# Optimization experiments

Measured on AMD Instinct MI355X. Metric: run time of the kernel, lower is better.

Reference implementation:

```python
import jax, jax.numpy as jnp
import numpy as np
from jax import lax

B, T, V, E, H, K = 128, 512, 100000, 100, 128, 12
HD = H // 2
START, STOP = 10, 11
NEG = -10000.0


def setup_inputs() -> dict:
    key = jax.random.key(0)
    ks = jax.random.split(key, 16)
    sentences = jax.random.randint(ks[0], (B, T), 0, V)
    embed = jax.random.normal(ks[1], (V, E), dtype=jnp.float32) * 0.1
    s = 1.0 / np.sqrt(HD).astype(np.float32)
    def u(k, shape):
        return jax.random.uniform(k, shape, minval=-s, maxval=s, dtype=jnp.float32)
    W_ih_f = u(ks[2], (4 * HD, E)); W_hh_f = u(ks[3], (4 * HD, HD))
    b_ih_f = u(ks[4], (4 * HD,));   b_hh_f = u(ks[5], (4 * HD,))
    W_ih_b = u(ks[6], (4 * HD, E)); W_hh_b = u(ks[7], (4 * HD, HD))
    b_ih_b = u(ks[8], (4 * HD,));   b_hh_b = u(ks[9], (4 * HD,))
    W_out = u(ks[10], (K, H)); b_out = u(ks[11], (K,))
    transitions = jax.random.normal(ks[12], (K, K), dtype=jnp.float32)
    transitions = transitions.at[:, START].set(NEG).at[STOP, :].set(NEG)
    h0 = jax.random.normal(ks[13], (2, B, HD), dtype=jnp.float32)
    c0 = jax.random.normal(ks[14], (2, B, HD), dtype=jnp.float32)
    return dict(sentences=sentences, embed=embed,
                W_ih_f=W_ih_f, W_hh_f=W_hh_f, b_ih_f=b_ih_f, b_hh_f=b_hh_f,
                W_ih_b=W_ih_b, W_hh_b=W_hh_b, b_ih_b=b_ih_b, b_hh_b=b_hh_b,
                W_out=W_out, b_out=b_out, transitions=transitions, h0=h0, c0=c0)


def _lstm_dir(x, h, c, Wih, Whh, bih, bhh):
    # x: [B,T,E] -> pre-gates [B,T,4HD] (input projection done once, outside scan)
    xg = jnp.einsum('bte,ge->btg', x, Wih) + bih + bhh
    def step(carry, xt):
        h, c = carry
        g = xt + h @ Whh.T                      # [B,4HD], gate order i,f,g,o (PyTorch)
        i, f, gg, o = jnp.split(g, 4, axis=-1)
        c = jax.nn.sigmoid(f) * c + jax.nn.sigmoid(i) * jnp.tanh(gg)
        h = jax.nn.sigmoid(o) * jnp.tanh(c)
        return (h, c), h
    _, hs = lax.scan(step, (h, c), jnp.swapaxes(xg, 0, 1))  # [T,B,HD]
    return jnp.swapaxes(hs, 0, 1)


def reference(sentences, embed, W_ih_f, W_hh_f, b_ih_f, b_hh_f,
              W_ih_b, W_hh_b, b_ih_b, b_hh_b, W_out, b_out,
              transitions, h0, c0):
    emb = embed[sentences]                       # [B,T,E]
    out_f = _lstm_dir(emb, h0[0], c0[0], W_ih_f, W_hh_f, b_ih_f, b_hh_f)
    out_b = _lstm_dir(emb[:, ::-1], h0[1], c0[1], W_ih_b, W_hh_b, b_ih_b, b_hh_b)[:, ::-1]
    feats = jnp.concatenate([out_f, out_b], axis=-1)   # [B,T,H]
    emissions = feats @ W_out.T + b_out                # [B,T,K]

    def viterbi(em):                                   # em: [T,K]
        def step(prev, e_t):
            v = prev[:, None] + transitions            # [K,K]: from-tag rows, to-tag cols
            return e_t + jnp.max(v, axis=0), jnp.argmax(v, axis=0)
        last, bps = lax.scan(step, em[0], em[1:])      # trellis[0] = emissions[0]
        score = jnp.max(last)
        start = jnp.argmax(last)
        def back(cur, bp):
            return bp[cur], cur                        # emit tag at t, carry tag at t-1
        tag0, tail = lax.scan(back, start, bps, reverse=True)
        path = jnp.concatenate([tag0[None], tail])     # [T]
        return score, path

    scores, paths = jax.vmap(viterbi)(emissions)
    return scores, paths
```

## Files before the change

### kernel.cpp

```cpp
#include <hip/hip_runtime.h>
#include <hip/hip_bf16.h>

#define Bn 128
#define Tn 512
#define En 100
#define G4 256
#define Hn 128
#define Kn 12

typedef short bf16x8 __attribute__((ext_vector_type(8)));
typedef float f32x4 __attribute__((ext_vector_type(4)));

__device__ __forceinline__ void wg_barrier() {
  asm volatile("s_waitcnt lgkmcnt(0)" ::: "memory");
  __builtin_amdgcn_s_barrier();
  asm volatile("" ::: "memory");
}

__device__ __forceinline__ float exp2_hw(float x) {
  float r; asm("v_exp_f32 %0, %1" : "=v"(r) : "v"(x)); return r;
}
__device__ __forceinline__ float rcp_hw(float x) {
  float r; asm("v_rcp_f32 %0, %1" : "=v"(r) : "v"(x)); return r;
}
__device__ __forceinline__ float fast_tanh(float x) {
  return 1.0f - 2.0f * rcp_hw(1.0f + exp2_hw(x * 2.8853900817779268f));
}
__device__ __forceinline__ unsigned int pk2bf(float a, float b) {
  unsigned int ua = __float_as_uint(a); ua += 0x7FFFu + ((ua >> 16) & 1u);
  unsigned int ub = __float_as_uint(b); ub += 0x7FFFu + ((ub >> 16) & 1u);
  return (ua >> 16) | (ub & 0xFFFF0000u);
}

__global__ __launch_bounds__(256) void proj_kernel(
    const int* __restrict__ sent, const float* __restrict__ embed,
    const float* __restrict__ WihF, const float* __restrict__ WihB,
    const float* __restrict__ bihF, const float* __restrict__ bhhF,
    const float* __restrict__ bihB, const float* __restrict__ bhhB,
    float* __restrict__ xgF, float* __restrict__ xgB, int dirSel) {
  __shared__ __align__(16) unsigned short embS[64][128];
  __shared__ __align__(16) unsigned short wS[128][128];
  __shared__ float bias_s[128];
  const int tid = threadIdx.x;
  const int nhalf = blockIdx.y;
  const int dir = (dirSel >= 0) ? dirSel : (int)blockIdx.z;
  const float* Wih = dir ? WihB : WihF;
  const float* bih = dir ? bihB : bihF;
  const float* bhh = dir ? bhhB : bhhF;
  float* xg = dir ? xgB : xgF;
  const int n0 = blockIdx.x * 64;
  const int g0 = nhalf * 128;
  {
    const int t = tid >> 2, q = tid & 3;
    const int row = sent[n0 + t];
    const float* er = embed + (size_t)row * En;
    for (int c = q; c < 16; c += 4) {
      uint4 wv;
      if (c < 12) {
        const float4 f0 = *(const float4*)(er + 8 * c);
        const float4 f1 = *(const float4*)(er + 8 * c + 4);
        wv = make_uint4(pk2bf(f0.x, f0.y), pk2bf(f0.z, f0.w),
                        pk2bf(f1.x, f1.y), pk2bf(f1.z, f1.w));
      } else if (c == 12) {
        float f[8];
#pragma unroll
        for (int j = 0; j < 8; ++j) { const int e = 96 + j; f[j] = (e < En) ? er[e] : 0.f; }
        wv = make_uint4(pk2bf(f[0], f[1]), pk2bf(f[2], f[3]),
                        pk2bf(f[4], f[5]), pk2bf(f[6], f[7]));
      } else {
        wv = make_uint4(0, 0, 0, 0);
      }
      *(uint4*)&embS[t][8 * (c ^ (t & 7))] = wv;
    }
  }
  {
    const int r = tid >> 1, q = tid & 1;
    const float* wr = Wih + (size_t)(g0 + r) * En;
    for (int c = q; c < 16; c += 2) {
      uint4 wv;
      if (c < 12) {
        const float4 f0 = *(const float4*)(wr + 8 * c);
        const float4 f1 = *(const float4*)(wr + 8 * c + 4);
        wv = make_uint4(pk2bf(f0.x, f0.y), pk2bf(f0.z, f0.w),
                        pk2bf(f1.x, f1.y), pk2bf(f1.z, f1.w));
      } else if (c == 12) {
        float f[8];
#pragma unroll
        for (int j = 0; j < 8; ++j) { const int e = 96 + j; f[j] = (e < En) ? wr[e] : 0.f; }
        wv = make_uint4(pk2bf(f[0], f[1]), pk2bf(f[2], f[3]),
                        pk2bf(f[4], f[5]), pk2bf(f[6], f[7]));
      } else {
        wv = make_uint4(0, 0, 0, 0);
      }
      *(uint4*)&wS[r][8 * (c ^ (r & 7))] = wv;
    }
  }
  if (tid < 128) bias_s[tid] = bih[g0 + tid] + bhh[g0 + tid];
  __syncthreads();
  const int m = tid >> 6;
  const int lane = tid & 63;
  const int lr = lane & 15;
  const int lq = lane >> 4;
  const int t = 16 * m + lr;
  f32x4 acc[8] = {};
#pragma unroll
  for (int ks = 0; ks < 4; ++ks) {
    const int cs = 4 * ks + lq;
    const bf16x8 af = *(const bf16x8*)&embS[t][8 * (cs ^ (lr & 7))];
#pragma unroll
    for (int nt = 0; nt < 8; ++nt) {
      const int g = 16 * nt + lr;
      const bf16x8 bf = *(const bf16x8*)&wS[g][8 * (cs ^ (lr & 7))];
      acc[nt] = __builtin_amdgcn_mfma_f32_16x16x32_bf16(af, bf, acc[nt], 0, 0, 0);
    }
  }
  float* xbase = xg + (size_t)(n0 + 16 * m) * G4 + g0;
#pragma unroll
  for (int nt = 0; nt < 8; ++nt) {
    const int g = 16 * nt + lr;
    const float bv = bias_s[g];
#pragma unroll
    for (int j = 0; j < 4; ++j) {
      const int tok = 4 * lq + j;
      xbase[(size_t)tok * G4 + g] = acc[nt][j] + bv;
    }
  }
}

__global__ __launch_bounds__(512, 2) void lstm_kernel(
    const float* __restrict__ xgF, const float* __restrict__ xgB,
    const float* __restrict__ WhhF, const float* __restrict__ WhhB,
    const float* __restrict__ h0, const float* __restrict__ c0,
    float* __restrict__ feats, int dirSel) {
  __shared__ __align__(16) float h_s[2][64];
  int d, b;
  if (dirSel < 0) { d = blockIdx.x >> 7; b = blockIdx.x & 127; }
  else            { d = dirSel;          b = blockIdx.x; }
  const int tid = threadIdx.x;
  const int lane = tid & 63;
  const int w = tid >> 6;
  const int kh = lane >> 5;
  const int gt = (lane >> 3) & 3;
  const int u = lane & 7;
  const int unit = 8 * w + u;
  const int row = gt * 64 + unit;
  const float* xg = d ? xgB : xgF;
  const float* Whh = d ? WhhB : WhhF;
  float a00,a01,a02,a03,a04,a05,a06,a07,a08,a09,a10,a11,a12,a13,a14,a15,
        a16,a17,a18,a19,a20,a21,a22,a23,a24,a25,a26,a27,a28,a29,a30,a31;
  {
    const float4* wp = (const float4*)(Whh + (size_t)row * 64 + 32 * kh);
    const float4 w0 = wp[0], w1 = wp[1], w2 = wp[2], w3 = wp[3];
    const float4 w4 = wp[4], w5 = wp[5], w6 = wp[6], w7 = wp[7];
#define ST(A, V) asm volatile("v_accvgpr_write_b32 %0, %1" : "=a"(A) : "v"(V))
    ST(a00, w0.x); ST(a01, w0.y); ST(a02, w0.z); ST(a03, w0.w);
    ST(a04, w1.x); ST(a05, w1.y); ST(a06, w1.z); ST(a07, w1.w);
    ST(a08, w2.x); ST(a09, w2.y); ST(a10, w2.z); ST(a11, w2.w);
    ST(a12, w3.x); ST(a13, w3.y); ST(a14, w3.z); ST(a15, w3.w);
    ST(a16, w4.x); ST(a17, w4.y); ST(a18, w4.z); ST(a19, w4.w);
    ST(a20, w5.x); ST(a21, w5.y); ST(a22, w5.z); ST(a23, w5.w);
    ST(a24, w6.x); ST(a25, w6.y); ST(a26, w6.z); ST(a27, w6.w);
    ST(a28, w7.x); ST(a29, w7.y); ST(a30, w7.z); ST(a31, w7.w);
#undef ST
  }
  const bool isT = (gt == 2);
  const float fA = isT ? 1.0f : 0.0f;
  const float fB = isT ? -2.0f : 1.0f;
  const float fC = isT ? 2.8853900817779268f : -1.4426950408889634f;
  float c = 0.f;
  if (lane < 8) {
    c = c0[(size_t)d * (Bn * 64) + (size_t)b * 64 + unit];
    h_s[0][unit] = h0[(size_t)d * (Bn * 64) + (size_t)b * 64 + unit];
  }
  const float* xb = xg + (size_t)b * Tn * G4 + row;
  float* fbase = feats + (size_t)b * Tn * Hn + d * 64 + unit;
  const int t0 = d ? (Tn - 1) : 0;
  const int ts = d ? -1 : 1;
  float p0 = 0.f, p1 = 0.f, p2 = 0.f, p3 = 0.f;
  if (kh == 0) {
    p0 = xb[(size_t)t0 * G4];
    p1 = xb[(size_t)(t0 + ts) * G4];
    p2 = xb[(size_t)(t0 + 2 * ts) * G4];
    p3 = xb[(size_t)(t0 + 3 * ts) * G4];
  }

#define ARD8(U0,U1,U2,U3,U4,U5,U6,U7, A0,A1,A2,A3,A4,A5,A6,A7)                \
  asm volatile("v_accvgpr_read_b32 %0, %8\n\t"                                \
               "v_accvgpr_read_b32 %1, %9\n\t"                                \
               "v_accvgpr_read_b32 %2, %10\n\t"                               \
               "v_accvgpr_read_b32 %3, %11\n\t"                               \
               "v_accvgpr_read_b32 %4, %12\n\t"                               \
               "v_accvgpr_read_b32 %5, %13\n\t"                               \
               "v_accvgpr_read_b32 %6, %14\n\t"                               \
               "v_accvgpr_read_b32 %7, %15"                                   \
               : "=&v"(U0),"=&v"(U1),"=&v"(U2),"=&v"(U3),                     \
                 "=&v"(U4),"=&v"(U5),"=&v"(U6),"=&v"(U7)                      \
               : "a"(A0),"a"(A1),"a"(A2),"a"(A3),                             \
                 "a"(A4),"a"(A5),"a"(A6),"a"(A7))
#define F4(HV, U0, U1, U2, U3)                                                 \
    s0 = fmaf((HV).x, U0, s0); s1 = fmaf((HV).y, U1, s1);                      \
    s2 = fmaf((HV).z, U2, s2); s3 = fmaf((HV).w, U3, s3);

#define LSTM_STEP(P, TT, RB) do {                                              \
    wg_barrier();                                                              \
    const float4* hp = (const float4*)(&h_s[RB][32 * kh]);                     \
    const float4 h0v = hp[0], h1v = hp[1], h2v = hp[2], h3v = hp[3];           \
    const float4 h4v = hp[4], h5v = hp[5], h6v = hp[6], h7v = hp[7];           \
    float u00,u01,u02,u03,u04,u05,u06,u07,u08,u09,u10,u11,u12,u13,u14,u15,     \
          u16,u17,u18,u19,u20,u21,u22,u23,u24,u25,u26,u27,u28,u29,u30,u31;     \
    ARD8(u00,u01,u02,u03,u04,u05,u06,u07, a00,a01,a02,a03,a04,a05,a06,a07);    \
    ARD8(u08,u09,u10,u11,u12,u13,u14,u15, a08,a09,a10,a11,a12,a13,a14,a15);    \
    ARD8(u16,u17,u18,u19,u20,u21,u22,u23, a16,a17,a18,a19,a20,a21,a22,a23);    \
    ARD8(u24,u25,u26,u27,u28,u29,u30,u31, a24,a25,a26,a27,a28,a29,a30,a31);    \
    float s0 = 0.f, s1 = 0.f, s2 = 0.f, s3 = 0.f;                              \
    F4(h0v, u00,u01,u02,u03)                                                   \
    F4(h1v, u04,u05,u06,u07)                                                   \
    F4(h2v, u08,u09,u10,u11)                                                   \
    F4(h3v, u12,u13,u14,u15)                                                   \
    F4(h4v, u16,u17,u18,u19)                                                   \
    F4(h5v, u20,u21,u22,u23)                                                   \
    F4(h6v, u24,u25,u26,u27)                                                   \
    F4(h7v, u28,u29,u30,u31)                                                   \
    const float smine = (s0 + s1) + (s2 + s3);                                 \
    const float stot = smine + __shfl_xor(smine, 32);                          \
    const float accv = (P) + stot;                                             \
    const float act = fmaf(fB, rcp_hw(1.0f + exp2_hw(fC * accv)), fA);         \
    const float gF = __shfl_xor(act, 8);                                       \
    const float gG = __shfl_xor(act, 16);                                      \
    const float gO = __shfl_xor(act, 24);                                      \
    if (lane < 8) {                                                            \
      c = fmaf(gF, c, act * gG);                                               \
      const float hh = gO * fast_tanh(c);                                      \
      h_s[RB ^ 1][unit] = hh;                                                  \
      fbase[(size_t)(TT) * Hn] = hh;                                           \
    }                                                                          \
  } while (0)

  for (int s = 0; s < Tn; s += 4) {
    const int tA = t0 + s * ts;
    LSTM_STEP(p0, tA, 0);
    if (kh == 0 && s + 4 < Tn) p0 = xb[(size_t)(t0 + (s + 4) * ts) * G4];
    LSTM_STEP(p1, tA + ts, 1);
    if (kh == 0 && s + 5 < Tn) p1 = xb[(size_t)(t0 + (s + 5) * ts) * G4];
    LSTM_STEP(p2, tA + 2 * ts, 0);
    if (kh == 0 && s + 6 < Tn) p2 = xb[(size_t)(t0 + (s + 6) * ts) * G4];
    LSTM_STEP(p3, tA + 3 * ts, 1);
    if (kh == 0 && s + 7 < Tn) p3 = xb[(size_t)(t0 + (s + 7) * ts) * G4];
  }
#undef LSTM_STEP
#undef F4
#undef ARD8
}

__global__ __launch_bounds__(256) void emis_kernel(
    const float* __restrict__ feats, const float* __restrict__ Wout,
    const float* __restrict__ bout, float* __restrict__ em) {
  __shared__ __align__(16) float Wo[Kn * Hn];
  __shared__ float bo[Kn];
  const int tid = threadIdx.x;
  for (int i = tid; i < Kn * Hn; i += 256) Wo[i] = Wout[i];
  if (tid < Kn) bo[tid] = bout[tid];
  __syncthreads();
  const int n = blockIdx.x * 256 + tid;
  float acc[Kn];
#pragma unroll
  for (int k = 0; k < Kn; ++k) acc[k] = bo[k];
  const float4* fp = (const float4*)(feats + (size_t)n * Hn);
#pragma unroll 4
  for (int d4 = 0; d4 < 32; ++d4) {
    const float4 v = fp[d4];
#pragma unroll
    for (int k = 0; k < Kn; ++k) {
      const float4 w = *(const float4*)&Wo[k * Hn + d4 * 4];
      acc[k] = fmaf(v.x, w.x, acc[k]);
      acc[k] = fmaf(v.y, w.y, acc[k]);
      acc[k] = fmaf(v.z, w.z, acc[k]);
      acc[k] = fmaf(v.w, w.w, acc[k]);
    }
  }
  float* ep = em + (size_t)n * Kn;
#pragma unroll
  for (int k = 0; k < Kn; k += 4)
    *(float4*)&ep[k] = make_float4(acc[k], acc[k + 1], acc[k + 2], acc[k + 3]);
}

#define AMAX(v, a, v2, a2) { if ((v2) > (v)) { (v) = (v2); (a) = (a2); } }

__global__ __launch_bounds__(64) void viterbi_kernel(
    const float* __restrict__ em, const float* __restrict__ trans,
    float* __restrict__ out) {
  __shared__ __align__(16) float em_s[Tn * Kn];
  __shared__ float trans_s[Kn * Kn];
  __shared__ unsigned char bp[(Tn - 1) * Kn];
  __shared__ short path_s[Tn];
  const int tid = threadIdx.x;
  const int b = blockIdx.x;
  {
    const float4* ebv = (const float4*)(em + (size_t)b * Tn * Kn);
    float4* emv = (float4*)em_s;
    for (int i = tid; i < (Tn * Kn) / 4; i += 64) emv[i] = ebv[i];
  }
  for (int i = tid; i < Kn * Kn; i += 64) trans_s[i] = trans[i];
  __syncthreads();
  const int lane = (tid < Kn) ? tid : 0;
  float treg[Kn];
#pragma unroll
  for (int f = 0; f < Kn; ++f) treg[f] = trans_s[f * Kn + lane];
  float prev = em_s[lane];
  for (int t = 1; t < Tn; ++t) {
    float cv[Kn];
#pragma unroll
    for (int f = 0; f < Kn; ++f) cv[f] = __shfl(prev, f) + treg[f];
    float m0 = cv[0], m1 = cv[2], m2 = cv[4], m3 = cv[6], m4 = cv[8], m5 = cv[10];
    int a0 = 0, a1 = 2, a2 = 4, a3 = 6, a4 = 8, a5 = 10;
    AMAX(m0, a0, cv[1], 1);  AMAX(m1, a1, cv[3], 3);
    AMAX(m2, a2, cv[5], 5);  AMAX(m3, a3, cv[7], 7);
    AMAX(m4, a4, cv[9], 9);  AMAX(m5, a5, cv[11], 11);
    AMAX(m0, a0, m1, a1); AMAX(m2, a2, m3, a3); AMAX(m4, a4, m5, a5);
    AMAX(m0, a0, m2, a2); AMAX(m0, a0, m4, a4);
    prev = em_s[t * Kn + lane] + m0;
    if (tid < Kn) bp[(t - 1) * Kn + tid] = (unsigned char)a0;
  }
  float fv[Kn];
#pragma unroll
  for (int f = 0; f < Kn; ++f) fv[f] = __shfl(prev, f);
  float m0 = fv[0], m1 = fv[2], m2 = fv[4], m3 = fv[6], m4 = fv[8], m5 = fv[10];
  int a0 = 0, a1 = 2, a2 = 4, a3 = 6, a4 = 8, a5 = 10;
  AMAX(m0, a0, fv[1], 1);  AMAX(m1, a1, fv[3], 3);
  AMAX(m2, a2, fv[5], 5);  AMAX(m3, a3, fv[7], 7);
  AMAX(m4, a4, fv[9], 9);  AMAX(m5, a5, fv[11], 11);
  AMAX(m0, a0, m1, a1); AMAX(m2, a2, m3, a3); AMAX(m4, a4, m5, a5);
  AMAX(m0, a0, m2, a2); AMAX(m0, a0, m4, a4);
  __syncthreads();
  if (tid == 0) {
    out[b] = m0;
    int cur = a0;
    for (int i = Tn - 2; i >= 0; --i) {
      path_s[i + 1] = (short)cur;
      cur = bp[i * Kn + cur];
    }
    path_s[0] = (short)cur;
  }
  __syncthreads();
  for (int i = tid; i < Tn; i += 64)
    out[Bn + (size_t)b * Tn + i] = (float)path_s[i];
}

extern "C" void kernel_launch(void* const* d_in, const int* in_sizes, int n_in,
                              void* d_out, int out_size, void* d_ws, size_t ws_size,
                              hipStream_t stream) {
  const int*   sent  = (const int*)d_in[0];
  const float* embed = (const float*)d_in[1];
  const float* Wih_f = (const float*)d_in[2];
  const float* Whh_f = (const float*)d_in[3];
  const float* bih_f = (const float*)d_in[4];
  const float* bhh_f = (const float*)d_in[5];
  const float* Wih_b = (const float*)d_in[6];
  const float* Whh_b = (const float*)d_in[7];
  const float* bih_b = (const float*)d_in[8];
  const float* bhh_b = (const float*)d_in[9];
  const float* Wout  = (const float*)d_in[10];
  const float* bout  = (const float*)d_in[11];
  const float* trans = (const float*)d_in[12];
  const float* h0    = (const float*)d_in[13];
  const float* c0    = (const float*)d_in[14];
  float* out = (float*)d_out;

  char* ws = (char*)d_ws;
  const size_t xgBytes   = (size_t)Bn * Tn * G4 * sizeof(float);
  const size_t featBytes = (size_t)Bn * Tn * Hn * sizeof(float);
  const size_t emBytes   = (size_t)Bn * Tn * Kn * sizeof(float);
  const int tokBlocks = (Bn * Tn) / 64;

  if (ws_size >= 2 * xgBytes + featBytes + emBytes) {
    float* xgF   = (float*)ws;
    float* xgB   = (float*)(ws + xgBytes);
    float* feats = (float*)(ws + 2 * xgBytes);
    float* emis  = (float*)(ws + 2 * xgBytes + featBytes);
    proj_kernel<<<dim3(tokBlocks, 2, 2), 256, 0, stream>>>(
        sent, embed, Wih_f, Wih_b, bih_f, bhh_f, bih_b, bhh_b, xgF, xgB, -1);
    lstm_kernel<<<256, 512, 0, stream>>>(xgF, xgB, Whh_f, Whh_b, h0, c0, feats, -1);
    emis_kernel<<<256, 256, 0, stream>>>(feats, Wout, bout, emis);
    viterbi_kernel<<<128, 64, 0, stream>>>(emis, trans, out);
  } else {
    float* xgS   = (float*)ws;
    float* feats = (float*)(ws + xgBytes);
    float* emis  = (float*)(ws + xgBytes + featBytes);
    proj_kernel<<<dim3(tokBlocks, 2, 1), 256, 0, stream>>>(
        sent, embed, Wih_f, Wih_b, bih_f, bhh_f, bih_b, bhh_b, xgS, xgS, 0);
    lstm_kernel<<<128, 512, 0, stream>>>(xgS, xgS, Whh_f, Whh_f, h0, c0, feats, 0);
    proj_kernel<<<dim3(tokBlocks, 2, 1), 256, 0, stream>>>(
        sent, embed, Wih_f, Wih_b, bih_f, bhh_f, bih_b, bhh_b, xgS, xgS, 1);
    lstm_kernel<<<128, 512, 0, stream>>>(xgS, xgS, Whh_b, Whh_b, h0, c0, feats, 1);
    emis_kernel<<<256, 256, 0, stream>>>(feats, Wout, bout, emis);
    viterbi_kernel<<<128, 64, 0, stream>>>(emis, trans, out);
  }
}
```

Measured before the change: 408.4 us.

## Batch 16 sequences per block and compute LSTM recurrence with bf16 MFMA

```diff
diff --git a/kernel.cpp b/kernel.cpp
--- a/kernel.cpp
+++ b/kernel.cpp
@@ -23,6 +23,9 @@
 __device__ __forceinline__ float rcp_hw(float x) {
   float r; asm("v_rcp_f32 %0, %1" : "=v"(r) : "v"(x)); return r;
 }
+__device__ __forceinline__ float fast_sigm(float x) {
+  return rcp_hw(1.0f + exp2_hw(x * -1.4426950408889634f));
+}
 __device__ __forceinline__ float fast_tanh(float x) {
   return 1.0f - 2.0f * rcp_hw(1.0f + exp2_hw(x * 2.8853900817779268f));
 }
@@ -30,6 +33,10 @@
   unsigned int ua = __float_as_uint(a); ua += 0x7FFFu + ((ua >> 16) & 1u);
   unsigned int ub = __float_as_uint(b); ub += 0x7FFFu + ((ub >> 16) & 1u);
   return (ua >> 16) | (ub & 0xFFFF0000u);
+}
+__device__ __forceinline__ unsigned short f2bf(float a) {
+  unsigned int ua = __float_as_uint(a); ua += 0x7FFFu + ((ua >> 16) & 1u);
+  return (unsigned short)(ua >> 16);
 }
 
 __global__ __launch_bounds__(256) void proj_kernel(
@@ -127,129 +134,106 @@
   }
 }
 
-__global__ __launch_bounds__(512, 2) void lstm_kernel(
+__global__ __launch_bounds__(256, 1) void lstm_mfma_kernel(
     const float* __restrict__ xgF, const float* __restrict__ xgB,
     const float* __restrict__ WhhF, const float* __restrict__ WhhB,
     const float* __restrict__ h0, const float* __restrict__ c0,
     float* __restrict__ feats, int dirSel) {
-  __shared__ __align__(16) float h_s[2][64];
-  int d, b;
-  if (dirSel < 0) { d = blockIdx.x >> 7; b = blockIdx.x & 127; }
-  else            { d = dirSel;          b = blockIdx.x; }
-  const int tid = threadIdx.x;
-  const int lane = tid & 63;
-  const int w = tid >> 6;
-  const int kh = lane >> 5;
-  const int gt = (lane >> 3) & 3;
-  const int u = lane & 7;
-  const int unit = 8 * w + u;
-  const int row = gt * 64 + unit;
+  __shared__ __align__(16) unsigned short wS[256 * 64];
+  __shared__ __align__(16) unsigned short hS[2][16 * 64];
+  const int d = (dirSel >= 0) ? dirSel : (int)blockIdx.y;
+  const int b0 = blockIdx.x * 16;
   const float* xg = d ? xgB : xgF;
   const float* Whh = d ? WhhB : WhhF;
-  float a00,a01,a02,a03,a04,a05,a06,a07,a08,a09,a10,a11,a12,a13,a14,a15,
-        a16,a17,a18,a19,a20,a21,a22,a23,a24,a25,a26,a27,a28,a29,a30,a31;
-  {
-    const float4* wp = (const float4*)(Whh + (size_t)row * 64 + 32 * kh);
-    const float4 w0 = wp[0], w1 = wp[1], w2 = wp[2], w3 = wp[3];
-    const float4 w4 = wp[4], w5 = wp[5], w6 = wp[6], w7 = wp[7];
-#define ST(A, V) asm volatile("v_accvgpr_write_b32 %0, %1" : "=a"(A) : "v"(V))
-    ST(a00, w0.x); ST(a01, w0.y); ST(a02, w0.z); ST(a03, w0.w);
-    ST(a04, w1.x); ST(a05, w1.y); ST(a06, w1.z); ST(a07, w1.w);
-    ST(a08, w2.x); ST(a09, w2.y); ST(a10, w2.z); ST(a11, w2.w);
-    ST(a12, w3.x); ST(a13, w3.y); ST(a14, w3.z); ST(a15, w3.w);
-    ST(a16, w4.x); ST(a17, w4.y); ST(a18, w4.z); ST(a19, w4.w);
-    ST(a20, w5.x); ST(a21, w5.y); ST(a22, w5.z); ST(a23, w5.w);
-    ST(a24, w6.x); ST(a25, w6.y); ST(a26, w6.z); ST(a27, w6.w);
-    ST(a28, w7.x); ST(a29, w7.y); ST(a30, w7.z); ST(a31, w7.w);
-#undef ST
-  }
-  const bool isT = (gt == 2);
-  const float fA = isT ? 1.0f : 0.0f;
-  const float fB = isT ? -2.0f : 1.0f;
-  const float fC = isT ? 2.8853900817779268f : -1.4426950408889634f;
-  float c = 0.f;
-  if (lane < 8) {
-    c = c0[(size_t)d * (Bn * 64) + (size_t)b * 64 + unit];
-    h_s[0][unit] = h0[(size_t)d * (Bn * 64) + (size_t)b * 64 + unit];
-  }
-  const float* xb = xg + (size_t)b * Tn * G4 + row;
-  float* fbase = feats + (size_t)b * Tn * Hn + d * 64 + unit;
+  const int tid = threadIdx.x;
+  const int w = tid >> 6;
+  const int lane = tid & 63;
+  const int cl = lane & 15;
+  const int lq = lane >> 4;
+  const int kk = 16 * w + cl;
+  {
+    const float* wr = Whh + (size_t)tid * 64;
+#pragma unroll
+    for (int s = 0; s < 8; ++s) {
+      const float4 f0 = *(const float4*)(wr + 8 * s);
+      const float4 f1 = *(const float4*)(wr + 8 * s + 4);
+      const uint4 v = make_uint4(pk2bf(f0.x, f0.y), pk2bf(f0.z, f0.w),
+                                 pk2bf(f1.x, f1.y), pk2bf(f1.z, f1.w));
+      *(uint4*)&wS[tid * 64 + (s ^ (tid & 7)) * 8] = v;
+    }
+  }
+  float c[4];
+#pragma unroll
+  for (int j = 0; j < 4; ++j) {
+    const int b = 4 * lq + j;
+    c[j] = c0[(size_t)d * (Bn * 64) + (size_t)(b0 + b) * 64 + kk];
+    const float hv = h0[(size_t)d * (Bn * 64) + (size_t)(b0 + b) * 64 + kk];
+    hS[0][b * 64 + (((kk >> 3) ^ (b & 7)) * 8) + (kk & 7)] = f2bf(hv);
+  }
+  __syncthreads();
+  bf16x8 bf00, bf01, bf10, bf11, bf20, bf21, bf30, bf31;
+  {
+#define LDB(A, CH) \
+    (*(const bf16x8*)&wS[(16 * (4 * (A) + w) + cl) * 64 + (((4 * (CH) + lq) ^ (cl & 7)) * 8)])
+    bf00 = LDB(0, 0); bf01 = LDB(0, 1);
+    bf10 = LDB(1, 0); bf11 = LDB(1, 1);
+    bf20 = LDB(2, 0); bf21 = LDB(2, 1);
+    bf30 = LDB(3, 0); bf31 = LDB(3, 1);
+#undef LDB
+  }
   const int t0 = d ? (Tn - 1) : 0;
   const int ts = d ? -1 : 1;
-  float p0 = 0.f, p1 = 0.f, p2 = 0.f, p3 = 0.f;
-  if (kh == 0) {
-    p0 = xb[(size_t)t0 * G4];
-    p1 = xb[(size_t)(t0 + ts) * G4];
-    p2 = xb[(size_t)(t0 + 2 * ts) * G4];
-    p3 = xb[(size_t)(t0 + 3 * ts) * G4];
-  }
-
-#define ARD8(U0,U1,U2,U3,U4,U5,U6,U7, A0,A1,A2,A3,A4,A5,A6,A7)                \
-  asm volatile("v_accvgpr_read_b32 %0, %8\n\t"                                \
-               "v_accvgpr_read_b32 %1, %9\n\t"                                \
-               "v_accvgpr_read_b32 %2, %10\n\t"                               \
-               "v_accvgpr_read_b32 %3, %11\n\t"                               \
-               "v_accvgpr_read_b32 %4, %12\n\t"                               \
-               "v_accvgpr_read_b32 %5, %13\n\t"                               \
-               "v_accvgpr_read_b32 %6, %14\n\t"                               \
-               "v_accvgpr_read_b32 %7, %15"                                   \
-               : "=&v"(U0),"=&v"(U1),"=&v"(U2),"=&v"(U3),                     \
-                 "=&v"(U4),"=&v"(U5),"=&v"(U6),"=&v"(U7)                      \
-               : "a"(A0),"a"(A1),"a"(A2),"a"(A3),                             \
-                 "a"(A4),"a"(A5),"a"(A6),"a"(A7))
-#define F4(HV, U0, U1, U2, U3)                                                 \
-    s0 = fmaf((HV).x, U0, s0); s1 = fmaf((HV).y, U1, s1);                      \
-    s2 = fmaf((HV).z, U2, s2); s3 = fmaf((HV).w, U3, s3);
-
-#define LSTM_STEP(P, TT, RB) do {                                              \
-    wg_barrier();                                                              \
-    const float4* hp = (const float4*)(&h_s[RB][32 * kh]);                     \
-    const float4 h0v = hp[0], h1v = hp[1], h2v = hp[2], h3v = hp[3];           \
-    const float4 h4v = hp[4], h5v = hp[5], h6v = hp[6], h7v = hp[7];           \
-    float u00,u01,u02,u03,u04,u05,u06,u07,u08,u09,u10,u11,u12,u13,u14,u15,     \
-          u16,u17,u18,u19,u20,u21,u22,u23,u24,u25,u26,u27,u28,u29,u30,u31;     \
-    ARD8(u00,u01,u02,u03,u04,u05,u06,u07, a00,a01,a02,a03,a04,a05,a06,a07);    \
-    ARD8(u08,u09,u10,u11,u12,u13,u14,u15, a08,a09,a10,a11,a12,a13,a14,a15);    \
-    ARD8(u16,u17,u18,u19,u20,u21,u22,u23, a16,a17,a18,a19,a20,a21,a22,a23);    \
-    ARD8(u24,u25,u26,u27,u28,u29,u30,u31, a24,a25,a26,a27,a28,a29,a30,a31);    \
-    float s0 = 0.f, s1 = 0.f, s2 = 0.f, s3 = 0.f;                              \
-    F4(h0v, u00,u01,u02,u03)                                                   \
-    F4(h1v, u04,u05,u06,u07)                                                   \
-    F4(h2v, u08,u09,u10,u11)                                                   \
-    F4(h3v, u12,u13,u14,u15)                                                   \
-    F4(h4v, u16,u17,u18,u19)                                                   \
-    F4(h5v, u20,u21,u22,u23)                                                   \
-    F4(h6v, u24,u25,u26,u27)                                                   \
-    F4(h7v, u28,u29,u30,u31)                                                   \
-    const float smine = (s0 + s1) + (s2 + s3);                                 \
-    const float stot = smine + __shfl_xor(smine, 32);                          \
-    const float accv = (P) + stot;                                             \
-    const float act = fmaf(fB, rcp_hw(1.0f + exp2_hw(fC * accv)), fA);         \
-    const float gF = __shfl_xor(act, 8);                                       \
-    const float gG = __shfl_xor(act, 16);                                      \
-    const float gO = __shfl_xor(act, 24);                                      \
-    if (lane < 8) {                                                            \
-      c = fmaf(gF, c, act * gG);                                               \
-      const float hh = gO * fast_tanh(c);                                      \
-      h_s[RB ^ 1][unit] = hh;                                                  \
-      fbase[(size_t)(TT) * Hn] = hh;                                           \
+  float* fbase = feats + (size_t)b0 * Tn * Hn + (size_t)d * 64 + kk;
+  float pA[4][4], pB[4][4];
+
+#define LOADXG(P, T) do {                                                      \
+    _Pragma("unroll")                                                          \
+    for (int a_ = 0; a_ < 4; ++a_) {                                           \
+      _Pragma("unroll")                                                        \
+      for (int j_ = 0; j_ < 4; ++j_) {                                         \
+        P[a_][j_] = xg[((size_t)(b0 + 4 * lq + j_) * Tn + (size_t)(T)) * G4    \
+                       + 16 * (4 * a_ + w) + cl];                              \
+      }                                                                        \
     }                                                                          \
   } while (0)
 
-  for (int s = 0; s < Tn; s += 4) {
+#define MF(AF, BF, ACC) \
+    ACC = __builtin_amdgcn_mfma_f32_16x16x32_bf16(AF, BF, ACC, 0, 0, 0)
+
+#define LSTM_STEP(PC, PN, T, RB, PF, TN) do {                                  \
+    wg_barrier();                                                              \
+    const bf16x8 af0 = *(const bf16x8*)&hS[RB][cl * 64 + ((lq ^ (cl & 7)) * 8)];      \
+    const bf16x8 af1 = *(const bf16x8*)&hS[RB][cl * 64 + (((4 + lq) ^ (cl & 7)) * 8)];\
+    if (PF) LOADXG(PN, TN);                                                    \
+    f32x4 ac0 = {}, ac1 = {}, ac2 = {}, ac3 = {};                              \
+    MF(af0, bf00, ac0); MF(af1, bf01, ac0);                                    \
+    MF(af0, bf10, ac1); MF(af1, bf11, ac1);                                    \
+    MF(af0, bf20, ac2); MF(af1, bf21, ac2);                                    \
+    MF(af0, bf30, ac3); MF(af1, bf31, ac3);                                    \
+    _Pragma("unroll")                                                          \
+    for (int j = 0; j < 4; ++j) {                                              \
+      const float ii = fast_sigm(ac0[j] + PC[0][j]);                           \
+      const float ff = fast_sigm(ac1[j] + PC[1][j]);                           \
+      const float gg = fast_tanh(ac2[j] + PC[2][j]);                           \
+      const float oo = fast_sigm(ac3[j] + PC[3][j]);                           \
+      c[j] = fmaf(ff, c[j], ii * gg);                                          \
+      const float hh = oo * fast_tanh(c[j]);                                   \
+      const int bb = 4 * lq + j;                                               \
+      fbase[(size_t)bb * Tn * Hn + (size_t)(T) * Hn] = hh;                     \
+      hS[(RB) ^ 1][bb * 64 + (((kk >> 3) ^ (bb & 7)) * 8) + (kk & 7)] = f2bf(hh); \
+    }                                                                          \
+  } while (0)
+
+  LOADXG(pA, t0);
+  for (int s = 0; s < Tn; s += 2) {
     const int tA = t0 + s * ts;
-    LSTM_STEP(p0, tA, 0);
-    if (kh == 0 && s + 4 < Tn) p0 = xb[(size_t)(t0 + (s + 4) * ts) * G4];
-    LSTM_STEP(p1, tA + ts, 1);
-    if (kh == 0 && s + 5 < Tn) p1 = xb[(size_t)(t0 + (s + 5) * ts) * G4];
-    LSTM_STEP(p2, tA + 2 * ts, 0);
-    if (kh == 0 && s + 6 < Tn) p2 = xb[(size_t)(t0 + (s + 6) * ts) * G4];
-    LSTM_STEP(p3, tA + 3 * ts, 1);
-    if (kh == 0 && s + 7 < Tn) p3 = xb[(size_t)(t0 + (s + 7) * ts) * G4];
+    const int tB = tA + ts;
+    LSTM_STEP(pA, pB, tA, 0, 1, tB);
+    LSTM_STEP(pB, pA, tB, 1, (s + 2 < Tn), tB + ts);
   }
 #undef LSTM_STEP
-#undef F4
-#undef ARD8
+#undef MF
+#undef LOADXG
 }
 
 __global__ __launch_bounds__(256) void emis_kernel(
@@ -379,7 +363,8 @@
     float* emis  = (float*)(ws + 2 * xgBytes + featBytes);
     proj_kernel<<<dim3(tokBlocks, 2, 2), 256, 0, stream>>>(
         sent, embed, Wih_f, Wih_b, bih_f, bhh_f, bih_b, bhh_b, xgF, xgB, -1);
-    lstm_kernel<<<256, 512, 0, stream>>>(xgF, xgB, Whh_f, Whh_b, h0, c0, feats, -1);
+    lstm_mfma_kernel<<<dim3(8, 2), 256, 0, stream>>>(
+        xgF, xgB, Whh_f, Whh_b, h0, c0, feats, -1);
     emis_kernel<<<256, 256, 0, stream>>>(feats, Wout, bout, emis);
     viterbi_kernel<<<128, 64, 0, stream>>>(emis, trans, out);
   } else {
@@ -388,10 +373,12 @@
     float* emis  = (float*)(ws + xgBytes + featBytes);
     proj_kernel<<<dim3(tokBlocks, 2, 1), 256, 0, stream>>>(
         sent, embed, Wih_f, Wih_b, bih_f, bhh_f, bih_b, bhh_b, xgS, xgS, 0);
-    lstm_kernel<<<128, 512, 0, stream>>>(xgS, xgS, Whh_f, Whh_f, h0, c0, feats, 0);
+    lstm_mfma_kernel<<<dim3(8, 1), 256, 0, stream>>>(
+        xgS, xgS, Whh_f, Whh_f, h0, c0, feats, 0);
     proj_kernel<<<dim3(tokBlocks, 2, 1), 256, 0, stream>>>(
         sent, embed, Wih_f, Wih_b, bih_f, bhh_f, bih_b, bhh_b, xgS, xgS, 1);
-    lstm_kernel<<<128, 512, 0, stream>>>(xgS, xgS, Whh_b, Whh_b, h0, c0, feats, 1);
+    lstm_mfma_kernel<<<dim3(8, 1), 256, 0, stream>>>(
+        xgS, xgS, Whh_b, Whh_b, h0, c0, feats, 1);
     emis_kernel<<<256, 256, 0, stream>>>(feats, Wout, bout, emis);
     viterbi_kernel<<<128, 64, 0, stream>>>(emis, trans, out);
   }
```

Measured after the change: 534.0 us. 30.7% more time.
